# Kernel tuning notes

Hardware: AMD Instinct MI355X
Metric: run time of the kernel (lower is better)

Reference implementation:

```python
import jax, jax.numpy as jnp
import numpy as np

N = 16384          # number of points (single graph, batch all-zero)
K = 20             # kNN neighbors (DynamicEdgeConv k=20), includes self like torch_cluster.knn
FEATURE_DIM = 128


def setup_inputs() -> dict:
    key = jax.random.key(0)
    ks = jax.random.split(key, 6)
    def lin(k, fan_in, fan_out):
        return (jax.random.normal(k, (fan_in, fan_out), dtype=jnp.float32)
                / np.float32(np.sqrt(fan_in)))
    return {
        "pos": jax.random.normal(ks[0], (N, 3), dtype=jnp.float32),
        "W1": lin(ks[1], 3, 64),    "b1": jnp.zeros((64,), jnp.float32),
        "We1": lin(ks[2], 128, 128), "be1": jnp.zeros((128,), jnp.float32),
        "We2": lin(ks[3], 256, 256), "be2": jnp.zeros((256,), jnp.float32),
        "W2": lin(ks[4], 256, FEATURE_DIM), "b2": jnp.zeros((FEATURE_DIM,), jnp.float32),
    }


def _knn_idx(x, k):
    # kNN graph on current features; indices are non-differentiable (as in PyG).
    x = jax.lax.stop_gradient(x)
    sq = jnp.sum(x * x, axis=-1)                      # [N]
    d2 = sq[:, None] - 2.0 * (x @ x.T) + sq[None, :]  # [N,N] squared distances
    _, idx = jax.lax.top_k(-d2, k)                    # [N,k], self included (d=0)
    return idx


def _edge_conv(x, W, b, k):
    # DynamicEdgeConv: message = MLP([x_i, x_j - x_i]), aggr = max over neighbors
    idx = _knn_idx(x, k)                              # [N,k]
    xj = x[idx]                                       # [N,k,F] gather
    xi = jnp.broadcast_to(x[:, None, :], xj.shape)    # [N,k,F]
    feat = jnp.concatenate([xi, xj - xi], axis=-1)    # [N,k,2F]
    h = jax.nn.relu(feat @ W + b)                     # [N,k,out]
    return jnp.max(h, axis=1)                         # [N,out]


def reference(pos, W1, b1, We1, be1, We2, be2, W2, b2):
    x = jax.nn.relu(pos @ W1 + b1)        # mlp1: 3 -> 64
    x = _edge_conv(x, We1, be1, K)        # lfa1: 2*64 -> 128
    x = _edge_conv(x, We2, be2, K)        # lfa2: 2*128 -> 256
    return x @ W2 + b2                    # mlp2: 256 -> feature_dim
```

## Files before the change

### kernel.cpp

```cpp
#include <hip/hip_runtime.h>
#include <hip/hip_bf16.h>

#define N_PTS 16384
#define KNN   20
#define LIST  32

typedef unsigned int u32;
typedef const __attribute__((address_space(1))) u32 glob_u32;
typedef __attribute__((address_space(3))) u32 lds_u32;

typedef __attribute__((ext_vector_type(8))) short bf16x8;
typedef __attribute__((ext_vector_type(4))) float f32x4;

__device__ __forceinline__ void g2lds16(const void* g, void* l) {
  __builtin_amdgcn_global_load_lds((glob_u32*)g, (lds_u32*)l, 16, 0, 0);
}

template<int F, int ROWS>
__device__ __forceinline__ void stage_c(const ushort* __restrict__ X, int row0, ushort* dst) {
  constexpr int NCH = F / 8;
  constexpr int TOT = ROWS * NCH;
  const int tid = threadIdx.x;
  const int wv = tid >> 6, ln = tid & 63;
#pragma unroll
  for (int base = 0; base < TOT; base += 256) {
    int g = base + wv * 64 + ln;
    int r = g / NCH;
    int p = g & (NCH - 1);
    int sc = p ^ (r & (NCH - 1));
    g2lds16(X + (size_t)(row0 + r) * F + sc * 8,
            dst + (size_t)(base + wv * 64) * 8);
  }
}

template<int F>
__device__ __forceinline__ bf16x8 ldfrag(const ushort* buf, int rbase, int kc, int ln) {
  constexpr int NCH = F / 8;
  int r  = rbase + (ln & 15);
  int pc = kc * 4 + (ln >> 4);
  int sp = pc ^ (r & (NCH - 1));
  return *(const bf16x8*)(buf + (size_t)r * F + sp * 8);
}

template<int F>
__global__ __launch_bounds__(256) void knn_kernel(const ushort* __restrict__ Xh,
                                                  const ushort* __restrict__ Xl,
                                                  const float* __restrict__ sqn,
                                                  int* __restrict__ out_cand) {
  constexpr int KC = F / 32;
  constexpr int NC = N_PTS / 2;
  constexpr int TS = 32;
  constexpr int NT = NC / TS;
  extern __shared__ ushort lds_raw[];
  ushort* cb  = lds_raw;
  float*  Bs  = (float*)(cb + 4 * TS * F);
  ushort* Bi  = (ushort*)(Bs + 64 * LIST);
  float*  Ld  = (float*)(Bi + 64 * LIST);
  ushort* Li  = (ushort*)(Ld + 64 * LIST);

  const int tid = threadIdx.x;
  const int wv = tid >> 6, ln = tid & 63;
  const int q0 = (blockIdx.x >> 1) * 64;
  const int hf = blockIdx.x & 1;
  const int cbase = hf * NC;

#pragma unroll
  for (int k = 0; k < 16; ++k) {
    int row = (wv * 16 + k) * LIST;
    if (ln < LIST) { Ld[row + ln] = 3.0e38f; Li[row + ln] = 0; }
  }
  float thr_reg = 3.0e38f;
  float myth[4];
#pragma unroll
  for (int r = 0; r < 4; ++r) myth[r] = 3.0e38f;
  int bcnt = 0;

  auto merge_q = [&](int qk) {
    int cnt = __shfl(bcnt, qk);
    int lrow = (wv * 16 + qk) * LIST;
    float key; int id;
    if (ln < 32) { key = Ld[lrow + ln]; id = (int)Li[lrow + ln]; }
    else {
      int j = ln - 32;
      bool v = j < cnt;
      key = v ? Bs[lrow + j] : 3.0e38f;
      id  = v ? (int)Bi[lrow + j] : 65535;
    }
#pragma unroll
    for (int kk = 2; kk <= 64; kk <<= 1) {
#pragma unroll
      for (int jj = kk >> 1; jj > 0; jj >>= 1) {
        float ok = __shfl_xor(key, jj);
        int   oi = __shfl_xor(id, jj);
        bool pless = (ok < key) || (ok == key && oi < id);
        bool take = pless == (((ln & jj) == 0) == ((ln & kk) == 0));
        key = take ? ok : key;
        id  = take ? oi : id;
      }
    }
    if (ln < 32) { Ld[lrow + ln] = key; Li[lrow + ln] = (ushort)id; }
    float tnew = __shfl(key, 31);
    thr_reg = (ln == qk) ? tnew : thr_reg;
    bcnt    = (ln == qk) ? 0 : bcnt;
  };

  stage_c<F, 64>(Xh, q0, cb);
  stage_c<F, 64>(Xl, q0, cb + 64 * F);
  __syncthreads();
  bf16x8 ah[KC], al[KC];
#pragma unroll
  for (int kc = 0; kc < KC; ++kc) {
    ah[kc] = ldfrag<F>(cb, wv * 16, kc, ln);
    al[kc] = ldfrag<F>(cb + 64 * F, wv * 16, kc, ln);
  }
  __syncthreads();
  stage_c<F, TS>(Xh, cbase, cb);
  stage_c<F, TS>(Xl, cbase, cb + TS * F);
  __syncthreads();

  for (int t = 0; t < NT; ++t) {
    const int c0 = t * TS;
    float cn[2];
#pragma unroll
    for (int cg = 0; cg < 2; ++cg) cn[cg] = sqn[cbase + c0 + cg * 16 + (ln & 15)];

    if (t + 1 < NT) {
      ushort* nb = cb + (size_t)((t + 1) & 1) * (2 * TS * F);
      stage_c<F, TS>(Xh, cbase + (t + 1) * TS, nb);
      stage_c<F, TS>(Xl, cbase + (t + 1) * TS, nb + TS * F);
    }

    const ushort* hi = cb + (size_t)(t & 1) * (2 * TS * F);
    const ushort* lo = hi + TS * F;

    f32x4 aH[2], aX[2];
#pragma unroll
    for (int cg = 0; cg < 2; ++cg) { aH[cg] = (f32x4){0,0,0,0}; aX[cg] = (f32x4){0,0,0,0}; }
#pragma unroll
    for (int kc = 0; kc < KC; ++kc) {
      bf16x8 bh0 = ldfrag<F>(hi, 0,  kc, ln);
      bf16x8 bh1 = ldfrag<F>(hi, 16, kc, ln);
      bf16x8 bl0 = ldfrag<F>(lo, 0,  kc, ln);
      bf16x8 bl1 = ldfrag<F>(lo, 16, kc, ln);
      aH[0] = __builtin_amdgcn_mfma_f32_16x16x32_bf16(ah[kc], bh0, aH[0], 0, 0, 0);
      aH[1] = __builtin_amdgcn_mfma_f32_16x16x32_bf16(ah[kc], bh1, aH[1], 0, 0, 0);
      aX[0] = __builtin_amdgcn_mfma_f32_16x16x32_bf16(al[kc], bh0, aX[0], 0, 0, 0);
      aX[1] = __builtin_amdgcn_mfma_f32_16x16x32_bf16(al[kc], bh1, aX[1], 0, 0, 0);
      aX[0] = __builtin_amdgcn_mfma_f32_16x16x32_bf16(ah[kc], bl0, aX[0], 0, 0, 0);
      aX[1] = __builtin_amdgcn_mfma_f32_16x16x32_bf16(ah[kc], bl1, aX[1], 0, 0, 0);
    }

#pragma unroll
    for (int cg = 0; cg < 2; ++cg) {
#pragma unroll
      for (int r = 0; r < 4; ++r) {
        float s = cn[cg] - 2.0f * (aH[cg][r] + aX[cg][r]);
        unsigned long long m = __ballot(s < myth[r]);
        if (m) {
          int qk = ((ln & 48) >> 2) + r;
          int basec = __shfl(bcnt, qk);
          if (s < myth[r]) {
            int pos = basec +
                __popcll(m & (0xFFFFull << (ln & 48)) & ((1ull << ln) - 1));
            int brow = (wv * 16 + qk) * LIST;
            Bs[brow + pos] = s;
            Bi[brow + pos] = (ushort)(cbase + c0 + cg * 16 + (ln & 15));
          }
          if (ln < 16 && (ln & 3) == r)
            bcnt += __popcll((m >> ((ln >> 2) * 16)) & 0xFFFFull);
        }
      }
      unsigned long long mm = __ballot(ln < 16 && bcnt > 16);
      if (mm) {
        do {
          int qk = __ffsll(mm) - 1;
          mm &= mm - 1;
          merge_q(qk);
        } while (mm);
#pragma unroll
        for (int rr = 0; rr < 4; ++rr) myth[rr] = __shfl(thr_reg, ((ln & 48) >> 2) + rr);
      }
    }
    __syncthreads();
  }

  {
    unsigned long long mm = __ballot(ln < 16 && bcnt > 0);
    while (mm) {
      int qk = __ffsll(mm) - 1;
      mm &= mm - 1;
      merge_q(qk);
    }
  }

#pragma unroll 1
  for (int k = 0; k < 16; ++k) {
    int q = wv * 16 + k;
    if (ln < LIST)
      out_cand[(size_t)(q0 + q) * (2 * LIST) + hf * LIST + ln] = (int)Li[q * LIST + ln];
  }
}

template<int F>
__global__ __launch_bounds__(256) void refine_kernel(const float* __restrict__ X,
                                                     const float* __restrict__ sqn,
                                                     const int* __restrict__ cand,
                                                     int* __restrict__ out_idx) {
  const int wv = threadIdx.x >> 6, ln = threadIdx.x & 63;
  const int q = blockIdx.x * 4 + wv;
  int ci = cand[(size_t)q * (2 * LIST) + ln];
  const float* qrow = X + (size_t)q * F;
  const float* crow = X + (size_t)ci * F;
  float dot = 0.f;
#pragma unroll
  for (int d = 0; d < F; d += 4) {
    float4 qv = *(const float4*)(qrow + d);
    float4 cv = *(const float4*)(crow + d);
    dot += qv.x * cv.x + qv.y * cv.y + qv.z * cv.z + qv.w * cv.w;
  }
  float s = sqn[ci] - 2.0f * dot;
  int rank = 0;
#pragma unroll 1
  for (int j = 0; j < 64; ++j) {
    float sj = __shfl(s, j);
    int   cj = __shfl(ci, j);
    rank += (sj < s) || (sj == s && cj < ci);
  }
  bool win = rank < KNN;
  unsigned long long wm = __ballot(win);
  int pos = __popcll(wm & ((1ull << ln) - 1));
  if (win) out_idx[(size_t)q * KNN + pos] = ci;
}

__global__ __launch_bounds__(256) void mlp1_kernel(const float* __restrict__ pos,
                                                   const float* __restrict__ W1,
                                                   const float* __restrict__ b1,
                                                   float* __restrict__ x1,
                                                   ushort* __restrict__ xh,
                                                   ushort* __restrict__ xl,
                                                   float* __restrict__ sqn) {
  int i = blockIdx.x * 4 + (threadIdx.x >> 6);
  int o = threadIdx.x & 63;
  float p0 = pos[i * 3], p1 = pos[i * 3 + 1], p2 = pos[i * 3 + 2];
  float v = p0 * W1[o] + p1 * W1[64 + o] + p2 * W1[128 + o] + b1[o];
  v = fmaxf(v, 0.f);
  x1[(size_t)i * 64 + o] = v;
  __hip_bfloat16 h = __float2bfloat16(v);
  float hv = __bfloat162float(h);
  __hip_bfloat16 l2 = __float2bfloat16(v - hv);
  xh[(size_t)i * 64 + o] = *(ushort*)&h;
  xl[(size_t)i * 64 + o] = *(ushort*)&l2;
  float ss = v * v;
#pragma unroll
  for (int d = 32; d; d >>= 1) ss += __shfl_xor(ss, d);
  if (o == 0) sqn[i] = ss;
}

template<int F>
__global__ __launch_bounds__(256) void prep_kernel(const float* __restrict__ x,
                                                   ushort* __restrict__ xh,
                                                   ushort* __restrict__ xl,
                                                   float* __restrict__ sqn) {
  int i = blockIdx.x * 4 + (threadIdx.x >> 6);
  int l = threadIdx.x & 63;
  float ss = 0.f;
#pragma unroll
  for (int d = l; d < F; d += 64) {
    float v = x[(size_t)i * F + d];
    ss += v * v;
    __hip_bfloat16 h = __float2bfloat16(v);
    float hv = __bfloat162float(h);
    __hip_bfloat16 l2 = __float2bfloat16(v - hv);
    xh[(size_t)i * F + d] = *(ushort*)&h;
    xl[(size_t)i * F + d] = *(ushort*)&l2;
  }
#pragma unroll
  for (int d = 32; d; d >>= 1) ss += __shfl_xor(ss, d);
  if (l == 0) sqn[i] = ss;
}

template<int K, int OUT, bool BIAS>
__global__ __launch_bounds__(256) void lin_kernel(const float* __restrict__ X,
                                                  const float* __restrict__ W,
                                                  const float* __restrict__ bias,
                                                  float* __restrict__ C) {
  constexpr int XD = OUT / 4;
  constexpr int YD = 256 / XD;
  constexpr int R = YD * 4;
  __shared__ float xs[R * K];
  const int tid = threadIdx.x;
  const int tx = tid % XD, ty = tid / XD;
  const size_t r0 = (size_t)blockIdx.x * R;
  const float4* Xv = (const float4*)(X + r0 * K);
  float4* xsv = (float4*)xs;
#pragma unroll
  for (int i2 = tid; i2 < R * K / 4; i2 += 256) xsv[i2] = Xv[i2];
  __syncthreads();
  float4 acc[4];
#pragma unroll
  for (int i = 0; i < 4; i++) acc[i] = make_float4(0.f, 0.f, 0.f, 0.f);
  const float4* W4 = (const float4*)W;
#pragma unroll 8
  for (int k = 0; k < K; ++k) {
    float4 wv = W4[k * XD + tx];
#pragma unroll
    for (int i = 0; i < 4; i++) {
      float xv = xs[(ty * 4 + i) * K + k];
      acc[i].x += xv * wv.x; acc[i].y += xv * wv.y;
      acc[i].z += xv * wv.z; acc[i].w += xv * wv.w;
    }
  }
  float4 bv = make_float4(0.f, 0.f, 0.f, 0.f);
  if (BIAS) bv = ((const float4*)bias)[tx];
#pragma unroll
  for (int i = 0; i < 4; i++) {
    float4 o;
    o.x = acc[i].x + bv.x; o.y = acc[i].y + bv.y;
    o.z = acc[i].z + bv.z; o.w = acc[i].w + bv.w;
    ((float4*)(C + (r0 + ty * 4 + i) * OUT))[tx] = o;
  }
}

template<int OUT>
__global__ void maxpool_kernel(const float* __restrict__ P, const float* __restrict__ Q,
                               const int* __restrict__ idx, float* __restrict__ xo) {
  __shared__ int nb[KNN];
  int i = blockIdx.x;
  if (threadIdx.x < KNN) nb[threadIdx.x] = idx[(size_t)i * KNN + threadIdx.x];
  __syncthreads();
  int o = threadIdx.x;
  float m = -3.0e38f;
#pragma unroll
  for (int j = 0; j < KNN; j++) m = fmaxf(m, Q[(size_t)nb[j] * OUT + o]);
  float p = P[(size_t)i * OUT + o];
  xo[(size_t)i * OUT + o] = fmaxf(p + m, 0.f);
}

__global__ void wsub_kernel(const float* __restrict__ We, float* __restrict__ Wp, int total) {
  int t = blockIdx.x * 256 + threadIdx.x;
  if (t < total) Wp[t] = We[t] - We[total + t];
}

extern "C" void kernel_launch(void* const* d_in, const int* in_sizes, int n_in,
                              void* d_out, int out_size, void* d_ws, size_t ws_size,
                              hipStream_t stream) {
  const float* pos = (const float*)d_in[0];
  const float* W1  = (const float*)d_in[1];
  const float* b1  = (const float*)d_in[2];
  const float* We1 = (const float*)d_in[3];
  const float* be1 = (const float*)d_in[4];
  const float* We2 = (const float*)d_in[5];
  const float* be2 = (const float*)d_in[6];
  const float* W2  = (const float*)d_in[7];
  const float* b2  = (const float*)d_in[8];
  float* out = (float*)d_out;

  const size_t N = N_PTS;
  float* ws  = (float*)d_ws;
  float* x1  = ws;
  float* P1  = x1 + N * 64;
  float* Q1  = P1 + N * 128;
  float* x2  = Q1 + N * 128;
  float* P2  = x2 + N * 128;
  float* Q2  = P2 + N * 256;
  float* x3  = Q2 + N * 256;
  float* sqn = x3 + N * 256;
  float* Wp1 = sqn + N;
  float* Wp2 = Wp1 + 64 * 128;
  int* idx1  = (int*)(Wp2 + 128 * 256);
  int* idx2  = idx1 + N * KNN;
  int* cand  = idx2 + N * KNN;
  ushort* X1h = (ushort*)(cand + N * 2 * LIST);
  ushort* X1l = X1h + N * 64;
  ushort* X2h = X1l + N * 64;
  ushort* X2l = X2h + N * 128;
  size_t need = (size_t)((char*)(X2l + N * 128) - (char*)d_ws);
  if (ws_size < need) return;

  auto lds_bytes = [](int F) {
    return (size_t)(4 * 32 * F) * 2 +
           (size_t)(64 * LIST) * 4 + (size_t)(64 * LIST) * 2 +
           (size_t)(64 * LIST) * 4 + (size_t)(64 * LIST) * 2;
  };
  size_t lds64 = lds_bytes(64), lds128 = lds_bytes(128);
  hipFuncSetAttribute(reinterpret_cast<const void*>(&knn_kernel<64>),
                      hipFuncAttributeMaxDynamicSharedMemorySize, (int)lds64);
  hipFuncSetAttribute(reinterpret_cast<const void*>(&knn_kernel<128>),
                      hipFuncAttributeMaxDynamicSharedMemorySize, (int)lds128);

  wsub_kernel<<<(64 * 128 + 255) / 256, 256, 0, stream>>>(We1, Wp1, 64 * 128);
  wsub_kernel<<<(128 * 256 + 255) / 256, 256, 0, stream>>>(We2, Wp2, 128 * 256);

  mlp1_kernel<<<N / 4, 256, 0, stream>>>(pos, W1, b1, x1, X1h, X1l, sqn);
  knn_kernel<64><<<N / 32, 256, lds64, stream>>>(X1h, X1l, sqn, cand);
  refine_kernel<64><<<N / 4, 256, 0, stream>>>(x1, sqn, cand, idx1);
  lin_kernel<64, 128, true ><<<N / 32, 256, 0, stream>>>(x1, Wp1, be1, P1);
  lin_kernel<64, 128, false><<<N / 32, 256, 0, stream>>>(x1, We1 + 64 * 128, nullptr, Q1);
  maxpool_kernel<128><<<N, 128, 0, stream>>>(P1, Q1, idx1, x2);

  prep_kernel<128><<<N / 4, 256, 0, stream>>>(x2, X2h, X2l, sqn);
  knn_kernel<128><<<N / 32, 256, lds128, stream>>>(X2h, X2l, sqn, cand);
  refine_kernel<128><<<N / 4, 256, 0, stream>>>(x2, sqn, cand, idx2);
  lin_kernel<128, 256, true ><<<N / 16, 256, 0, stream>>>(x2, Wp2, be2, P2);
  lin_kernel<128, 256, false><<<N / 16, 256, 0, stream>>>(x2, We2 + 128 * 256, nullptr, Q2);
  maxpool_kernel<256><<<N, 256, 0, stream>>>(P2, Q2, idx2, x3);

  lin_kernel<256, 128, true ><<<N / 32, 256, 0, stream>>>(x3, W2, b2, out);
}
```

Before: 2.045 ms.

## Split kNN candidate range four ways and keep per-query lists in registers

The kNN kernel now divides the candidate set into four slices instead of two, doubling the grid so more blocks run concurrently. The per-query top-32 lists move from LDS into registers, with the merge unrolled over the 16 queries, which frees LDS for higher occupancy. The refine kernel now ranks 128 candidates, two per lane, and the candidate buffer aliases the Q2 workspace. The costs are more refine work, more register pressure from the unrolled merges, and a reliance on Q2 not being written before the second refine runs.

```diff
diff --git a/kernel.cpp b/kernel.cpp
--- a/kernel.cpp
+++ b/kernel.cpp
@@ -4,6 +4,7 @@
 #define N_PTS 16384
 #define KNN   20
 #define LIST  32
+#define NSPLIT 4
 
 typedef unsigned int u32;
 typedef const __attribute__((address_space(1))) u32 glob_u32;
@@ -48,61 +49,29 @@
                                                   const float* __restrict__ sqn,
                                                   int* __restrict__ out_cand) {
   constexpr int KC = F / 32;
-  constexpr int NC = N_PTS / 2;
+  constexpr int NC = N_PTS / NSPLIT;
   constexpr int TS = 32;
   constexpr int NT = NC / TS;
   extern __shared__ ushort lds_raw[];
   ushort* cb  = lds_raw;
   float*  Bs  = (float*)(cb + 4 * TS * F);
   ushort* Bi  = (ushort*)(Bs + 64 * LIST);
-  float*  Ld  = (float*)(Bi + 64 * LIST);
-  ushort* Li  = (ushort*)(Ld + 64 * LIST);
 
   const int tid = threadIdx.x;
   const int wv = tid >> 6, ln = tid & 63;
-  const int q0 = (blockIdx.x >> 1) * 64;
-  const int hf = blockIdx.x & 1;
+  const int q0 = (blockIdx.x >> 2) * 64;
+  const int hf = blockIdx.x & 3;
   const int cbase = hf * NC;
 
-#pragma unroll
-  for (int k = 0; k < 16; ++k) {
-    int row = (wv * 16 + k) * LIST;
-    if (ln < LIST) { Ld[row + ln] = 3.0e38f; Li[row + ln] = 0; }
-  }
+  float ld_d[16];
+  int   ld_i[16];
+#pragma unroll
+  for (int k = 0; k < 16; ++k) { ld_d[k] = 3.0e38f; ld_i[k] = 0; }
   float thr_reg = 3.0e38f;
   float myth[4];
 #pragma unroll
   for (int r = 0; r < 4; ++r) myth[r] = 3.0e38f;
   int bcnt = 0;
-
-  auto merge_q = [&](int qk) {
-    int cnt = __shfl(bcnt, qk);
-    int lrow = (wv * 16 + qk) * LIST;
-    float key; int id;
-    if (ln < 32) { key = Ld[lrow + ln]; id = (int)Li[lrow + ln]; }
-    else {
-      int j = ln - 32;
-      bool v = j < cnt;
-      key = v ? Bs[lrow + j] : 3.0e38f;
-      id  = v ? (int)Bi[lrow + j] : 65535;
-    }
-#pragma unroll
-    for (int kk = 2; kk <= 64; kk <<= 1) {
-#pragma unroll
-      for (int jj = kk >> 1; jj > 0; jj >>= 1) {
-        float ok = __shfl_xor(key, jj);
-        int   oi = __shfl_xor(id, jj);
-        bool pless = (ok < key) || (ok == key && oi < id);
-        bool take = pless == (((ln & jj) == 0) == ((ln & kk) == 0));
-        key = take ? ok : key;
-        id  = take ? oi : id;
-      }
-    }
-    if (ln < 32) { Ld[lrow + ln] = key; Li[lrow + ln] = (ushort)id; }
-    float tnew = __shfl(key, 31);
-    thr_reg = (ln == qk) ? tnew : thr_reg;
-    bcnt    = (ln == qk) ? 0 : bcnt;
-  };
 
   stage_c<F, 64>(Xh, q0, cb);
   stage_c<F, 64>(Xl, q0, cb + 64 * F);
@@ -172,11 +141,37 @@
       }
       unsigned long long mm = __ballot(ln < 16 && bcnt > 16);
       if (mm) {
-        do {
-          int qk = __ffsll(mm) - 1;
-          mm &= mm - 1;
-          merge_q(qk);
-        } while (mm);
+#pragma unroll
+        for (int k = 0; k < 16; ++k) {
+          if ((mm >> k) & 1) {
+            int cnt = __shfl(bcnt, k);
+            int brow = (wv * 16 + k) * LIST;
+            float key; int id;
+            if (ln < 32) { key = ld_d[k]; id = ld_i[k]; }
+            else {
+              int j = ln - 32;
+              bool v = j < cnt;
+              key = v ? Bs[brow + j] : 3.0e38f;
+              id  = v ? (int)Bi[brow + j] : 65535;
+            }
+#pragma unroll
+            for (int kk = 2; kk <= 64; kk <<= 1) {
+#pragma unroll
+              for (int jj = kk >> 1; jj > 0; jj >>= 1) {
+                float ok = __shfl_xor(key, jj);
+                int   oi = __shfl_xor(id, jj);
+                bool pless = (ok < key) || (ok == key && oi < id);
+                bool take = pless == (((ln & jj) == 0) == ((ln & kk) == 0));
+                key = take ? ok : key;
+                id  = take ? oi : id;
+              }
+            }
+            if (ln < 32) { ld_d[k] = key; ld_i[k] = id; }
+            float tnew = __shfl(key, 31);
+            thr_reg = (ln == k) ? tnew : thr_reg;
+            bcnt    = (ln == k) ? 0 : bcnt;
+          }
+        }
 #pragma unroll
         for (int rr = 0; rr < 4; ++rr) myth[rr] = __shfl(thr_reg, ((ln & 48) >> 2) + rr);
       }
@@ -186,18 +181,42 @@
 
   {
     unsigned long long mm = __ballot(ln < 16 && bcnt > 0);
-    while (mm) {
-      int qk = __ffsll(mm) - 1;
-      mm &= mm - 1;
-      merge_q(qk);
+    if (mm) {
+#pragma unroll
+      for (int k = 0; k < 16; ++k) {
+        if ((mm >> k) & 1) {
+          int cnt = __shfl(bcnt, k);
+          int brow = (wv * 16 + k) * LIST;
+          float key; int id;
+          if (ln < 32) { key = ld_d[k]; id = ld_i[k]; }
+          else {
+            int j = ln - 32;
+            bool v = j < cnt;
+            key = v ? Bs[brow + j] : 3.0e38f;
+            id  = v ? (int)Bi[brow + j] : 65535;
+          }
+#pragma unroll
+          for (int kk = 2; kk <= 64; kk <<= 1) {
+#pragma unroll
+            for (int jj = kk >> 1; jj > 0; jj >>= 1) {
+              float ok = __shfl_xor(key, jj);
+              int   oi = __shfl_xor(id, jj);
+              bool pless = (ok < key) || (ok == key && oi < id);
+              bool take = pless == (((ln & jj) == 0) == ((ln & kk) == 0));
+              key = take ? ok : key;
+              id  = take ? oi : id;
+            }
+          }
+          if (ln < 32) { ld_d[k] = key; ld_i[k] = id; }
+        }
+      }
     }
   }
 
-#pragma unroll 1
+#pragma unroll
   for (int k = 0; k < 16; ++k) {
-    int q = wv * 16 + k;
     if (ln < LIST)
-      out_cand[(size_t)(q0 + q) * (2 * LIST) + hf * LIST + ln] = (int)Li[q * LIST + ln];
+      out_cand[(size_t)(q0 + wv * 16 + k) * (NSPLIT * LIST) + hf * LIST + ln] = ld_i[k];
   }
 }
 
@@ -206,30 +225,35 @@
                                                      const float* __restrict__ sqn,
                                                      const int* __restrict__ cand,
                                                      int* __restrict__ out_idx) {
+  constexpr int CW = NSPLIT * LIST;
   const int wv = threadIdx.x >> 6, ln = threadIdx.x & 63;
   const int q = blockIdx.x * 4 + wv;
-  int ci = cand[(size_t)q * (2 * LIST) + ln];
+  int c0 = cand[(size_t)q * CW + ln];
+  int c1 = cand[(size_t)q * CW + 64 + ln];
   const float* qrow = X + (size_t)q * F;
-  const float* crow = X + (size_t)ci * F;
-  float dot = 0.f;
+  const float* crow0 = X + (size_t)c0 * F;
+  const float* crow1 = X + (size_t)c1 * F;
+  float dot0 = 0.f, dot1 = 0.f;
 #pragma unroll
   for (int d = 0; d < F; d += 4) {
     float4 qv = *(const float4*)(qrow + d);
-    float4 cv = *(const float4*)(crow + d);
-    dot += qv.x * cv.x + qv.y * cv.y + qv.z * cv.z + qv.w * cv.w;
-  }
-  float s = sqn[ci] - 2.0f * dot;
-  int rank = 0;
+    float4 v0 = *(const float4*)(crow0 + d);
+    float4 v1 = *(const float4*)(crow1 + d);
+    dot0 += qv.x * v0.x + qv.y * v0.y + qv.z * v0.z + qv.w * v0.w;
+    dot1 += qv.x * v1.x + qv.y * v1.y + qv.z * v1.z + qv.w * v1.w;
+  }
+  float s0 = sqn[c0] - 2.0f * dot0;
+  float s1 = sqn[c1] - 2.0f * dot1;
+  int rank0 = 0, rank1 = 0;
 #pragma unroll 1
   for (int j = 0; j < 64; ++j) {
-    float sj = __shfl(s, j);
-    int   cj = __shfl(ci, j);
-    rank += (sj < s) || (sj == s && cj < ci);
-  }
-  bool win = rank < KNN;
-  unsigned long long wm = __ballot(win);
-  int pos = __popcll(wm & ((1ull << ln) - 1));
-  if (win) out_idx[(size_t)q * KNN + pos] = ci;
+    float a0 = __shfl(s0, j); int i0 = __shfl(c0, j);
+    float a1 = __shfl(s1, j); int i1 = __shfl(c1, j);
+    rank0 += ((a0 < s0) || (a0 == s0 && i0 < c0)) + ((a1 < s0) || (a1 == s0 && i1 < c0));
+    rank1 += ((a0 < s1) || (a0 == s1 && i0 < c1)) + ((a1 < s1) || (a1 == s1 && i1 < c1));
+  }
+  if (rank0 < KNN) out_idx[(size_t)q * KNN + rank0] = c0;
+  if (rank1 < KNN) out_idx[(size_t)q * KNN + rank1] = c1;
 }
 
 __global__ __launch_bounds__(256) void mlp1_kernel(const float* __restrict__ pos,
@@ -369,8 +393,8 @@
   float* Wp2 = Wp1 + 64 * 128;
   int* idx1  = (int*)(Wp2 + 128 * 256);
   int* idx2  = idx1 + N * KNN;
-  int* cand  = idx2 + N * KNN;
-  ushort* X1h = (ushort*)(cand + N * 2 * LIST);
+  int* cand  = (int*)Q2;
+  ushort* X1h = (ushort*)(idx2 + N * KNN);
   ushort* X1l = X1h + N * 64;
   ushort* X2h = X1l + N * 64;
   ushort* X2l = X2h + N * 128;
@@ -379,7 +403,6 @@
 
   auto lds_bytes = [](int F) {
     return (size_t)(4 * 32 * F) * 2 +
-           (size_t)(64 * LIST) * 4 + (size_t)(64 * LIST) * 2 +
            (size_t)(64 * LIST) * 4 + (size_t)(64 * LIST) * 2;
   };
   size_t lds64 = lds_bytes(64), lds128 = lds_bytes(128);
@@ -392,14 +415,14 @@
   wsub_kernel<<<(128 * 256 + 255) / 256, 256, 0, stream>>>(We2, Wp2, 128 * 256);
 
   mlp1_kernel<<<N / 4, 256, 0, stream>>>(pos, W1, b1, x1, X1h, X1l, sqn);
-  knn_kernel<64><<<N / 32, 256, lds64, stream>>>(X1h, X1l, sqn, cand);
+  knn_kernel<64><<<(N / 64) * NSPLIT, 256, lds64, stream>>>(X1h, X1l, sqn, cand);
   refine_kernel<64><<<N / 4, 256, 0, stream>>>(x1, sqn, cand, idx1);
   lin_kernel<64, 128, true ><<<N / 32, 256, 0, stream>>>(x1, Wp1, be1, P1);
   lin_kernel<64, 128, false><<<N / 32, 256, 0, stream>>>(x1, We1 + 64 * 128, nullptr, Q1);
   maxpool_kernel<128><<<N, 128, 0, stream>>>(P1, Q1, idx1, x2);
 
   prep_kernel<128><<<N / 4, 256, 0, stream>>>(x2, X2h, X2l, sqn);
-  knn_kernel<128><<<N / 32, 256, lds128, stream>>>(X2h, X2l, sqn, cand);
+  knn_kernel<128><<<(N / 64) * NSPLIT, 256, lds128, stream>>>(X2h, X2l, sqn, cand);
   refine_kernel<128><<<N / 4, 256, 0, stream>>>(x2, sqn, cand, idx2);
   lin_kernel<128, 256, true ><<<N / 16, 256, 0, stream>>>(x2, Wp2, be2, P2);
   lin_kernel<128, 256, false><<<N / 16, 256, 0, stream>>>(x2, We2 + 128 * 256, nullptr, Q2);
```

Result: slower. 3.075 ms (+50.4%).

## Triple-buffer kNN candidate tiles with explicit vmcnt waits and LDS-staged norms

Applied to the files above, without the earlier changes.

Converts the kNN kernel's double-buffered candidate staging into a three-slot ring that prefetches two tiles ahead. Each iteration uses a raw s_barrier and an s_waitcnt vmcnt instead of a full __syncthreads. Candidate squared norms are also loaded into LDS asynchronously, replacing the per-tile global loads. Separately, the refine kernel writes winners directly at their rank slot rather than compacting with a ballot, which changes output ordering to sorted order. The goal is to hide global-load latency behind the MFMA and selection work, at the cost of more LDS and fragile hand-written waitcnt values.

```diff
diff --git a/kernel.cpp b/kernel.cpp
--- a/kernel.cpp
+++ b/kernel.cpp
@@ -14,6 +14,13 @@
 
 __device__ __forceinline__ void g2lds16(const void* g, void* l) {
   __builtin_amdgcn_global_load_lds((glob_u32*)g, (lds_u32*)l, 16, 0, 0);
+}
+
+template<int N>
+__device__ __forceinline__ void wait_vm() {
+  if constexpr (N == 0) asm volatile("s_waitcnt vmcnt(0)" ::: "memory");
+  else if constexpr (N == 3) asm volatile("s_waitcnt vmcnt(3)" ::: "memory");
+  else if constexpr (N == 5) asm volatile("s_waitcnt vmcnt(5)" ::: "memory");
 }
 
 template<int F, int ROWS>
@@ -51,9 +58,12 @@
   constexpr int NC = N_PTS / 2;
   constexpr int TS = 32;
   constexpr int NT = NC / TS;
+  constexpr int SLOT = 2 * TS * F;
+  constexpr int LPSN = F / 32 + 1;
   extern __shared__ ushort lds_raw[];
   ushort* cb  = lds_raw;
-  float*  Bs  = (float*)(cb + 4 * TS * F);
+  float* nlds = (float*)(cb + 3 * SLOT);
+  float*  Bs  = nlds + 96;
   ushort* Bi  = (ushort*)(Bs + 64 * LIST);
   float*  Ld  = (float*)(Bi + 64 * LIST);
   ushort* Li  = (ushort*)(Ld + 64 * LIST);
@@ -113,25 +123,35 @@
     ah[kc] = ldfrag<F>(cb, wv * 16, kc, ln);
     al[kc] = ldfrag<F>(cb + 64 * F, wv * 16, kc, ln);
   }
+  asm volatile("s_waitcnt lgkmcnt(0)" ::: "memory");
   __syncthreads();
-  stage_c<F, TS>(Xh, cbase, cb);
-  stage_c<F, TS>(Xl, cbase, cb + TS * F);
-  __syncthreads();
-
+
+#pragma unroll
+  for (int t0 = 0; t0 < 2; ++t0) {
+    const int row0 = cbase + t0 * TS;
+    stage_c<F, TS>(Xh, row0, cb + t0 * SLOT);
+    stage_c<F, TS>(Xl, row0, cb + t0 * SLOT + TS * F);
+    if (ln < 8) g2lds16(sqn + row0 + ln * 4, nlds + t0 * 32);
+  }
+  wait_vm<LPSN>();
+
+#pragma unroll 1
   for (int t = 0; t < NT; ++t) {
+    __builtin_amdgcn_s_barrier();
+    asm volatile("" ::: "memory");
+    if (t + 2 < NT) {
+      const int sl2 = (t + 2) % 3;
+      const int row0 = cbase + (t + 2) * TS;
+      stage_c<F, TS>(Xh, row0, cb + sl2 * SLOT);
+      stage_c<F, TS>(Xl, row0, cb + sl2 * SLOT + TS * F);
+      if (ln < 8) g2lds16(sqn + row0 + ln * 4, nlds + sl2 * 32);
+    }
+    const int sl = t % 3;
     const int c0 = t * TS;
-    float cn[2];
-#pragma unroll
-    for (int cg = 0; cg < 2; ++cg) cn[cg] = sqn[cbase + c0 + cg * 16 + (ln & 15)];
-
-    if (t + 1 < NT) {
-      ushort* nb = cb + (size_t)((t + 1) & 1) * (2 * TS * F);
-      stage_c<F, TS>(Xh, cbase + (t + 1) * TS, nb);
-      stage_c<F, TS>(Xl, cbase + (t + 1) * TS, nb + TS * F);
-    }
-
-    const ushort* hi = cb + (size_t)(t & 1) * (2 * TS * F);
+    const ushort* hi = cb + sl * SLOT;
     const ushort* lo = hi + TS * F;
+    float cn0 = nlds[sl * 32 + (ln & 15)];
+    float cn1 = nlds[sl * 32 + 16 + (ln & 15)];
 
     f32x4 aH[2], aX[2];
 #pragma unroll
@@ -154,7 +174,8 @@
     for (int cg = 0; cg < 2; ++cg) {
 #pragma unroll
       for (int r = 0; r < 4; ++r) {
-        float s = cn[cg] - 2.0f * (aH[cg][r] + aX[cg][r]);
+        float cnv = (cg == 0) ? cn0 : cn1;
+        float s = cnv - 2.0f * (aH[cg][r] + aX[cg][r]);
         unsigned long long m = __ballot(s < myth[r]);
         if (m) {
           int qk = ((ln & 48) >> 2) + r;
@@ -181,7 +202,8 @@
         for (int rr = 0; rr < 4; ++rr) myth[rr] = __shfl(thr_reg, ((ln & 48) >> 2) + rr);
       }
     }
-    __syncthreads();
+
+    if (t + 2 < NT) wait_vm<LPSN>(); else wait_vm<0>();
   }
 
   {
@@ -226,10 +248,7 @@
     int   cj = __shfl(ci, j);
     rank += (sj < s) || (sj == s && cj < ci);
   }
-  bool win = rank < KNN;
-  unsigned long long wm = __ballot(win);
-  int pos = __popcll(wm & ((1ull << ln) - 1));
-  if (win) out_idx[(size_t)q * KNN + pos] = ci;
+  if (rank < KNN) out_idx[(size_t)q * KNN + rank] = ci;
 }
 
 __global__ __launch_bounds__(256) void mlp1_kernel(const float* __restrict__ pos,
@@ -378,7 +397,7 @@
   if (ws_size < need) return;
 
   auto lds_bytes = [](int F) {
-    return (size_t)(4 * 32 * F) * 2 +
+    return (size_t)(3 * 2 * 32 * F) * 2 + 3 * 32 * 4 +
            (size_t)(64 * LIST) * 4 + (size_t)(64 * LIST) * 2 +
            (size_t)(64 * LIST) * 4 + (size_t)(64 * LIST) * 2;
   };
```

After: 2.137 ms. 4.5% more time.

## Restructure kNN into single-wave blocks with register-fed MFMA and four-way split

Applied to the files above, without the earlier changes.

The kNN kernel now uses 64-thread blocks. Each wave handles 32 queries against a quarter of the candidate set. Candidate fragments are loaded straight from global memory into double-buffered registers instead of being staged through swizzled LDS, which removes the block-wide barriers and LDS fragment reads. The refine kernel is widened to rank 128 candidates per query, and the candidate buffer is aliased onto an unused workspace region. In exchange there is more redundant global/L2 traffic, since each wave fetches candidates itself, and twice the refine work.

```diff
diff --git a/kernel.cpp b/kernel.cpp
--- a/kernel.cpp
+++ b/kernel.cpp
@@ -4,80 +4,63 @@
 #define N_PTS 16384
 #define KNN   20
 #define LIST  32
-
-typedef unsigned int u32;
-typedef const __attribute__((address_space(1))) u32 glob_u32;
-typedef __attribute__((address_space(3))) u32 lds_u32;
+#define NSPLIT 4
 
 typedef __attribute__((ext_vector_type(8))) short bf16x8;
 typedef __attribute__((ext_vector_type(4))) float f32x4;
 
-__device__ __forceinline__ void g2lds16(const void* g, void* l) {
-  __builtin_amdgcn_global_load_lds((glob_u32*)g, (lds_u32*)l, 16, 0, 0);
-}
-
-template<int F, int ROWS>
-__device__ __forceinline__ void stage_c(const ushort* __restrict__ X, int row0, ushort* dst) {
-  constexpr int NCH = F / 8;
-  constexpr int TOT = ROWS * NCH;
-  const int tid = threadIdx.x;
-  const int wv = tid >> 6, ln = tid & 63;
-#pragma unroll
-  for (int base = 0; base < TOT; base += 256) {
-    int g = base + wv * 64 + ln;
-    int r = g / NCH;
-    int p = g & (NCH - 1);
-    int sc = p ^ (r & (NCH - 1));
-    g2lds16(X + (size_t)(row0 + r) * F + sc * 8,
-            dst + (size_t)(base + wv * 64) * 8);
-  }
-}
-
 template<int F>
-__device__ __forceinline__ bf16x8 ldfrag(const ushort* buf, int rbase, int kc, int ln) {
-  constexpr int NCH = F / 8;
-  int r  = rbase + (ln & 15);
-  int pc = kc * 4 + (ln >> 4);
-  int sp = pc ^ (r & (NCH - 1));
-  return *(const bf16x8*)(buf + (size_t)r * F + sp * 8);
+__device__ __forceinline__ void load_B(const ushort* __restrict__ Xh,
+                                       const ushort* __restrict__ Xl,
+                                       const float* __restrict__ sqn,
+                                       int c0, int ln,
+                                       bf16x8 (&bh)[F / 32], bf16x8 (&bl)[F / 32],
+                                       float& cn) {
+  constexpr int KC = F / 32;
+  const int apc = ln >> 4;
+  size_t roff = (size_t)(c0 + (ln & 15)) * F;
+#pragma unroll
+  for (int kc = 0; kc < KC; ++kc) {
+    size_t off = roff + (size_t)(kc * 4 + apc) * 8;
+    bh[kc] = *(const bf16x8*)(Xh + off);
+    bl[kc] = *(const bf16x8*)(Xl + off);
+  }
+  cn = sqn[c0 + (ln & 15)];
 }
 
 template<int F>
-__global__ __launch_bounds__(256) void knn_kernel(const ushort* __restrict__ Xh,
-                                                  const ushort* __restrict__ Xl,
-                                                  const float* __restrict__ sqn,
-                                                  int* __restrict__ out_cand) {
+__global__ __launch_bounds__(64, 2) void knn_kernel(const ushort* __restrict__ Xh,
+                                                    const ushort* __restrict__ Xl,
+                                                    const float* __restrict__ sqn,
+                                                    int* __restrict__ out_cand) {
   constexpr int KC = F / 32;
-  constexpr int NC = N_PTS / 2;
-  constexpr int TS = 32;
+  constexpr int NC = N_PTS / NSPLIT;
+  constexpr int TS = 16;
   constexpr int NT = NC / TS;
-  extern __shared__ ushort lds_raw[];
-  ushort* cb  = lds_raw;
-  float*  Bs  = (float*)(cb + 4 * TS * F);
-  ushort* Bi  = (ushort*)(Bs + 64 * LIST);
-  float*  Ld  = (float*)(Bi + 64 * LIST);
-  ushort* Li  = (ushort*)(Ld + 64 * LIST);
-
-  const int tid = threadIdx.x;
-  const int wv = tid >> 6, ln = tid & 63;
-  const int q0 = (blockIdx.x >> 1) * 64;
-  const int hf = blockIdx.x & 1;
+  __shared__ float  Bs[32 * LIST];
+  __shared__ ushort Bi[32 * LIST];
+  __shared__ float  Ld[32 * LIST];
+  __shared__ ushort Li[32 * LIST];
+
+  const int ln = threadIdx.x;
+  const int q0 = (int)(blockIdx.x >> 2) * 32;
+  const int hf = blockIdx.x & 3;
   const int cbase = hf * NC;
 
 #pragma unroll
   for (int k = 0; k < 16; ++k) {
-    int row = (wv * 16 + k) * LIST;
-    if (ln < LIST) { Ld[row + ln] = 3.0e38f; Li[row + ln] = 0; }
+    int idx = k * 64 + ln;
+    Ld[idx] = 3.0e38f; Li[idx] = 0;
   }
   float thr_reg = 3.0e38f;
-  float myth[4];
-#pragma unroll
-  for (int r = 0; r < 4; ++r) myth[r] = 3.0e38f;
+  float myth[8];
+#pragma unroll
+  for (int i = 0; i < 8; ++i) myth[i] = 3.0e38f;
   int bcnt = 0;
 
   auto merge_q = [&](int qk) {
     int cnt = __shfl(bcnt, qk);
-    int lrow = (wv * 16 + qk) * LIST;
+    int lrow = qk * LIST;
     float key; int id;
     if (ln < 32) { key = Ld[lrow + ln]; id = (int)Li[lrow + ln]; }
     else {
@@ -104,88 +87,89 @@
     bcnt    = (ln == qk) ? 0 : bcnt;
   };
 
-  stage_c<F, 64>(Xh, q0, cb);
-  stage_c<F, 64>(Xl, q0, cb + 64 * F);
-  __syncthreads();
-  bf16x8 ah[KC], al[KC];
-#pragma unroll
-  for (int kc = 0; kc < KC; ++kc) {
-    ah[kc] = ldfrag<F>(cb, wv * 16, kc, ln);
-    al[kc] = ldfrag<F>(cb + 64 * F, wv * 16, kc, ln);
-  }
-  __syncthreads();
-  stage_c<F, TS>(Xh, cbase, cb);
-  stage_c<F, TS>(Xl, cbase, cb + TS * F);
-  __syncthreads();
-
-  for (int t = 0; t < NT; ++t) {
-    const int c0 = t * TS;
-    float cn[2];
-#pragma unroll
-    for (int cg = 0; cg < 2; ++cg) cn[cg] = sqn[cbase + c0 + cg * 16 + (ln & 15)];
-
-    if (t + 1 < NT) {
-      ushort* nb = cb + (size_t)((t + 1) & 1) * (2 * TS * F);
-      stage_c<F, TS>(Xh, cbase + (t + 1) * TS, nb);
-      stage_c<F, TS>(Xl, cbase + (t + 1) * TS, nb + TS * F);
-    }
-
-    const ushort* hi = cb + (size_t)(t & 1) * (2 * TS * F);
-    const ushort* lo = hi + TS * F;
-
+  bf16x8 ah[2][KC], al[2][KC];
+  {
+    const int apc = ln >> 4;
+#pragma unroll
+    for (int qg = 0; qg < 2; ++qg)
+#pragma unroll
+      for (int kc = 0; kc < KC; ++kc) {
+        size_t off = (size_t)(q0 + qg * 16 + (ln & 15)) * F + (size_t)(kc * 4 + apc) * 8;
+        ah[qg][kc] = *(const bf16x8*)(Xh + off);
+        al[qg][kc] = *(const bf16x8*)(Xl + off);
+      }
+  }
+
+  bf16x8 b0h[KC], b0l[KC], b1h[KC], b1l[KC];
+  float cn0, cn1;
+  load_B<F>(Xh, Xl, sqn, cbase, ln, b0h, b0l, cn0);
+  load_B<F>(Xh, Xl, sqn, cbase + TS, ln, b1h, b1l, cn1);
+
+  auto step = [&](bf16x8 (&bh)[KC], bf16x8 (&bl)[KC], float& cn, int t) {
     f32x4 aH[2], aX[2];
 #pragma unroll
-    for (int cg = 0; cg < 2; ++cg) { aH[cg] = (f32x4){0,0,0,0}; aX[cg] = (f32x4){0,0,0,0}; }
+    for (int qg = 0; qg < 2; ++qg) { aH[qg] = (f32x4){0,0,0,0}; aX[qg] = (f32x4){0,0,0,0}; }
 #pragma unroll
     for (int kc = 0; kc < KC; ++kc) {
-      bf16x8 bh0 = ldfrag<F>(hi, 0,  kc, ln);
-      bf16x8 bh1 = ldfrag<F>(hi, 16, kc, ln);
-      bf16x8 bl0 = ldfrag<F>(lo, 0,  kc, ln);
-      bf16x8 bl1 = ldfrag<F>(lo, 16, kc, ln);
-      aH[0] = __builtin_amdgcn_mfma_f32_16x16x32_bf16(ah[kc], bh0, aH[0], 0, 0, 0);
-      aH[1] = __builtin_amdgcn_mfma_f32_16x16x32_bf16(ah[kc], bh1, aH[1], 0, 0, 0);
-      aX[0] = __builtin_amdgcn_mfma_f32_16x16x32_bf16(al[kc], bh0, aX[0], 0, 0, 0);
-      aX[1] = __builtin_amdgcn_mfma_f32_16x16x32_bf16(al[kc], bh1, aX[1], 0, 0, 0);
-      aX[0] = __builtin_amdgcn_mfma_f32_16x16x32_bf16(ah[kc], bl0, aX[0], 0, 0, 0);
-      aX[1] = __builtin_amdgcn_mfma_f32_16x16x32_bf16(ah[kc], bl1, aX[1], 0, 0, 0);
-    }
-
-#pragma unroll
-    for (int cg = 0; cg < 2; ++cg) {
+#pragma unroll
+      for (int qg = 0; qg < 2; ++qg) {
+        aH[qg] = __builtin_amdgcn_mfma_f32_16x16x32_bf16(ah[qg][kc], bh[kc], aH[qg], 0, 0, 0);
+        aX[qg] = __builtin_amdgcn_mfma_f32_16x16x32_bf16(al[qg][kc], bh[kc], aX[qg], 0, 0, 0);
+        aX[qg] = __builtin_amdgcn_mfma_f32_16x16x32_bf16(ah[qg][kc], bl[kc], aX[qg], 0, 0, 0);
+      }
+    }
+    float s8[8];
+#pragma unroll
+    for (int qg = 0; qg < 2; ++qg)
+#pragma unroll
+      for (int r = 0; r < 4; ++r)
+        s8[qg * 4 + r] = cn - 2.0f * (aH[qg][r] + aX[qg][r]);
+
+    if (t + 2 < NT) load_B<F>(Xh, Xl, sqn, cbase + (t + 2) * TS, ln, bh, bl, cn);
+
+    const int ci = cbase + t * TS + (ln & 15);
+#pragma unroll
+    for (int qg = 0; qg < 2; ++qg)
 #pragma unroll
       for (int r = 0; r < 4; ++r) {
-        float s = cn[cg] - 2.0f * (aH[cg][r] + aX[cg][r]);
-        unsigned long long m = __ballot(s < myth[r]);
+        float s = s8[qg * 4 + r];
+        unsigned long long m = __ballot(s < myth[qg * 4 + r]);
         if (m) {
-          int qk = ((ln & 48) >> 2) + r;
+          int qk = qg * 16 + ((ln & 48) >> 2) + r;
           int basec = __shfl(bcnt, qk);
-          if (s < myth[r]) {
+          if (s < myth[qg * 4 + r]) {
             int pos = basec +
                 __popcll(m & (0xFFFFull << (ln & 48)) & ((1ull << ln) - 1));
-            int brow = (wv * 16 + qk) * LIST;
-            Bs[brow + pos] = s;
-            Bi[brow + pos] = (ushort)(cbase + c0 + cg * 16 + (ln & 15));
+            Bs[qk * LIST + pos] = s;
+            Bi[qk * LIST + pos] = (ushort)ci;
           }
-          if (ln < 16 && (ln & 3) == r)
-            bcnt += __popcll((m >> ((ln >> 2) * 16)) & 0xFFFFull);
+          if (ln < 32 && (ln >> 4) == qg && (ln & 3) == r)
+            bcnt += __popcll((m >> (((ln & 15) >> 2) * 16)) & 0xFFFFull);
         }
       }
-      unsigned long long mm = __ballot(ln < 16 && bcnt > 16);
-      if (mm) {
-        do {
-          int qk = __ffsll(mm) - 1;
-          mm &= mm - 1;
-          merge_q(qk);
-        } while (mm);
-#pragma unroll
-        for (int rr = 0; rr < 4; ++rr) myth[rr] = __shfl(thr_reg, ((ln & 48) >> 2) + rr);
-      }
-    }
-    __syncthreads();
+    unsigned long long mm = __ballot(ln < 32 && bcnt > 16);
+    if (mm) {
+      do {
+        int qk = __ffsll(mm) - 1;
+        mm &= mm - 1;
+        merge_q(qk);
+      } while (mm);
+#pragma unroll
+      for (int qg = 0; qg < 2; ++qg)
+#pragma unroll
+        for (int r = 0; r < 4; ++r)
+          myth[qg * 4 + r] = __shfl(thr_reg, qg * 16 + ((ln & 48) >> 2) + r);
+    }
+  };
+
+#pragma unroll 1
+  for (int t = 0; t < NT; t += 2) {
+    step(b0h, b0l, cn0, t);
+    step(b1h, b1l, cn1, t + 1);
   }
 
   {
-    unsigned long long mm = __ballot(ln < 16 && bcnt > 0);
+    unsigned long long mm = __ballot(ln < 32 && bcnt > 0);
     while (mm) {
       int qk = __ffsll(mm) - 1;
       mm &= mm - 1;
@@ -193,11 +177,11 @@
     }
   }
 
-#pragma unroll 1
-  for (int k = 0; k < 16; ++k) {
-    int q = wv * 16 + k;
-    if (ln < LIST)
-      out_cand[(size_t)(q0 + q) * (2 * LIST) + hf * LIST + ln] = (int)Li[q * LIST + ln];
+#pragma unroll
+  for (int k2 = 0; k2 < 16; ++k2) {
+    int row = k2 * 2 + (ln >> 5);
+    int col = ln & 31;
+    out_cand[(size_t)(q0 + row) * (NSPLIT * LIST) + hf * LIST + col] = (int)Li[row * LIST + col];
   }
 }
 
@@ -206,30 +190,35 @@
                                                      const float* __restrict__ sqn,
                                                      const int* __restrict__ cand,
                                                      int* __restrict__ out_idx) {
+  constexpr int CW = NSPLIT * LIST;
   const int wv = threadIdx.x >> 6, ln = threadIdx.x & 63;
   const int q = blockIdx.x * 4 + wv;
-  int ci = cand[(size_t)q * (2 * LIST) + ln];
+  int c0 = cand[(size_t)q * CW + ln];
+  int c1 = cand[(size_t)q * CW + 64 + ln];
   const float* qrow = X + (size_t)q * F;
-  const float* crow = X + (size_t)ci * F;
-  float dot = 0.f;
+  const float* crow0 = X + (size_t)c0 * F;
+  const float* crow1 = X + (size_t)c1 * F;
+  float dot0 = 0.f, dot1 = 0.f;
 #pragma unroll
   for (int d = 0; d < F; d += 4) {
     float4 qv = *(const float4*)(qrow + d);
-    float4 cv = *(const float4*)(crow + d);
-    dot += qv.x * cv.x + qv.y * cv.y + qv.z * cv.z + qv.w * cv.w;
-  }
-  float s = sqn[ci] - 2.0f * dot;
-  int rank = 0;
+    float4 v0 = *(const float4*)(crow0 + d);
+    float4 v1 = *(const float4*)(crow1 + d);
+    dot0 += qv.x * v0.x + qv.y * v0.y + qv.z * v0.z + qv.w * v0.w;
+    dot1 += qv.x * v1.x + qv.y * v1.y + qv.z * v1.z + qv.w * v1.w;
+  }
+  float s0 = sqn[c0] - 2.0f * dot0;
+  float s1 = sqn[c1] - 2.0f * dot1;
+  int rank0 = 0, rank1 = 0;
 #pragma unroll 1
   for (int j = 0; j < 64; ++j) {
-    float sj = __shfl(s, j);
-    int   cj = __shfl(ci, j);
-    rank += (sj < s) || (sj == s && cj < ci);
-  }
-  bool win = rank < KNN;
-  unsigned long long wm = __ballot(win);
-  int pos = __popcll(wm & ((1ull << ln) - 1));
-  if (win) out_idx[(size_t)q * KNN + pos] = ci;
+    float a0 = __shfl(s0, j); int i0 = __shfl(c0, j);
+    float a1 = __shfl(s1, j); int i1 = __shfl(c1, j);
+    rank0 += ((a0 < s0) || (a0 == s0 && i0 < c0)) + ((a1 < s0) || (a1 == s0 && i1 < c0));
+    rank1 += ((a0 < s1) || (a0 == s1 && i0 < c1)) + ((a1 < s1) || (a1 == s1 && i1 < c1));
+  }
+  if (rank0 < KNN) out_idx[(size_t)q * KNN + rank0] = c0;
+  if (rank1 < KNN) out_idx[(size_t)q * KNN + rank1] = c1;
 }
 
 __global__ __launch_bounds__(256) void mlp1_kernel(const float* __restrict__ pos,
@@ -369,37 +358,26 @@
   float* Wp2 = Wp1 + 64 * 128;
   int* idx1  = (int*)(Wp2 + 128 * 256);
   int* idx2  = idx1 + N * KNN;
-  int* cand  = idx2 + N * KNN;
-  ushort* X1h = (ushort*)(cand + N * 2 * LIST);
+  int* cand  = (int*)Q2;
+  ushort* X1h = (ushort*)(idx2 + N * KNN);
   ushort* X1l = X1h + N * 64;
   ushort* X2h = X1l + N * 64;
   ushort* X2l = X2h + N * 128;
   size_t need = (size_t)((char*)(X2l + N * 128) - (char*)d_ws);
   if (ws_size < need) return;
 
-  auto lds_bytes = [](int F) {
-    return (size_t)(4 * 32 * F) * 2 +
-           (size_t)(64 * LIST) * 4 + (size_t)(64 * LIST) * 2 +
-           (size_t)(64 * LIST) * 4 + (size_t)(64 * LIST) * 2;
-  };
-  size_t lds64 = lds_bytes(64), lds128 = lds_bytes(128);
-  hipFuncSetAttribute(reinterpret_cast<const void*>(&knn_kernel<64>),
-                      hipFuncAttributeMaxDynamicSharedMemorySize, (int)lds64);
-  hipFuncSetAttribute(reinterpret_cast<const void*>(&knn_kernel<128>),
-                      hipFuncAttributeMaxDynamicSharedMemorySize, (int)lds128);
-
   wsub_kernel<<<(64 * 128 + 255) / 256, 256, 0, stream>>>(We1, Wp1, 64 * 128);
   wsub_kernel<<<(128 * 256 + 255) / 256, 256, 0, stream>>>(We2, Wp2, 128 * 256);
 
   mlp1_kernel<<<N / 4, 256, 0, stream>>>(pos, W1, b1, x1, X1h, X1l, sqn);
-  knn_kernel<64><<<N / 32, 256, lds64, stream>>>(X1h, X1l, sqn, cand);
+  knn_kernel<64><<<(N / 32) * NSPLIT, 64, 0, stream>>>(X1h, X1l, sqn, cand);
   refine_kernel<64><<<N / 4, 256, 0, stream>>>(x1, sqn, cand, idx1);
   lin_kernel<64, 128, true ><<<N / 32, 256, 0, stream>>>(x1, Wp1, be1, P1);
   lin_kernel<64, 128, false><<<N / 32, 256, 0, stream>>>(x1, We1 + 64 * 128, nullptr, Q1);
   maxpool_kernel<128><<<N, 128, 0, stream>>>(P1, Q1, idx1, x2);
 
   prep_kernel<128><<<N / 4, 256, 0, stream>>>(x2, X2h, X2l, sqn);
-  knn_kernel<128><<<N / 32, 256, lds128, stream>>>(X2h, X2l, sqn, cand);
+  knn_kernel<128><<<(N / 32) * NSPLIT, 64, 0, stream>>>(X2h, X2l, sqn, cand);
   refine_kernel<128><<<N / 4, 256, 0, stream>>>(x2, sqn, cand, idx2);
   lin_kernel<128, 256, true ><<<N / 16, 256, 0, stream>>>(x2, Wp2, be2, P2);
   lin_kernel<128, 256, false><<<N / 16, 256, 0, stream>>>(x2, We2 + 128 * 256, nullptr, Q2);
```

New measurement: 2.125 ms. 3.9% more time.
